# Kernel tuning notes

Hardware: AMD Instinct MI355X
Metric: run time of the kernel (lower is better)

## Reference

```python
import jax, jax.numpy as jnp
import numpy as np

DIM = 512
HEADS = 8
HEAD_DIM = DIM // HEADS
EPS = 1e-6
LN_EPS = 1e-5


def setup_inputs() -> dict:
    key = jax.random.key(0)
    ks = jax.random.split(key, 7)
    B, S = 2, 2048
    std = 1.0 / np.sqrt(DIM)
    return {
        "x": jax.random.normal(ks[0], (B, S, DIM), dtype=jnp.float32),
        "Wq": jax.random.normal(ks[1], (DIM, DIM), dtype=jnp.float32) * std,
        "Wk": jax.random.normal(ks[2], (DIM, DIM), dtype=jnp.float32) * std,
        "Wv": jax.random.normal(ks[3], (DIM, DIM), dtype=jnp.float32) * std,
        "Wo": jax.random.normal(ks[4], (DIM, DIM), dtype=jnp.float32) * std,
        "ln_gamma": jnp.ones((DIM,), dtype=jnp.float32),
        "ln_beta": jnp.zeros((DIM,), dtype=jnp.float32),
    }


def _hardsigmoid(x):
    return jnp.clip(x / 6.0 + 0.5, 0.0, 1.0)


def _softshrink(x, lambd=0.5):
    return jnp.where(x > lambd, x - lambd, jnp.where(x < -lambd, x + lambd, 0.0))


def reference(x, Wq, Wk, Wv, Wo, ln_gamma, ln_beta):
    B, S, D = x.shape
    # torch Linear: y = x @ W.T
    q = (x @ Wq.T).reshape(B, S, HEADS, HEAD_DIM).transpose(0, 2, 1, 3)
    k = (x @ Wk.T).reshape(B, S, HEADS, HEAD_DIM).transpose(0, 2, 1, 3)
    v = (x @ Wv.T).reshape(B, S, HEADS, HEAD_DIM).transpose(0, 2, 1, 3)
    scale = 1.0 / np.sqrt(HEAD_DIM)
    scores = jnp.einsum("bhqd,bhkd->bhqk", q, k) * scale  # [B,H,S,S]
    attn_soft = jax.nn.softmax(scores, axis=-1)
    gated = attn_soft * _hardsigmoid(scores)
    attn_weights = gated / (gated.sum(axis=-1, keepdims=True) + EPS)
    attn_out = jnp.einsum("bhqk,bhkd->bhqd", attn_weights, v)
    attn_out = attn_out.transpose(0, 2, 1, 3).reshape(B, S, D)
    out = attn_out @ Wo.T
    out = out / (1.0 + jnp.abs(out))  # softsign
    out = out + _softshrink(x)
    # LayerNorm over last dim
    mu = out.mean(axis=-1, keepdims=True)
    var = ((out - mu) ** 2).mean(axis=-1, keepdims=True)
    out = (out - mu) * jax.lax.rsqrt(var + LN_EPS) * ln_gamma + ln_beta
    return out
```

## Files before the change

### kernel.cpp

```cpp
#include <hip/hip_runtime.h>

#define DIMD 512
#define NB 2
#define SEQ 2048
#define NHEADS 8
#define HDIM 64
#define MROWS (NB*SEQ)

typedef short s16x8 __attribute__((ext_vector_type(8)));
typedef float f32x4 __attribute__((ext_vector_type(4)));
typedef float f32x16 __attribute__((ext_vector_type(16)));
typedef unsigned short u16;
typedef unsigned int u32;

__device__ __forceinline__ u16 f2bf(float f) {
    union { float f; u32 u; } c; c.f = f;
    u32 u = c.u;
    return (u16)((u + 0x7FFFu + ((u >> 16) & 1u)) >> 16);
}
__device__ __forceinline__ float bf2f(u16 v) {
    union { u32 u; float f; } c; c.u = ((u32)v) << 16;
    return c.f;
}

__device__ __forceinline__ f32x4 mfma16(s16x8 a, s16x8 b, f32x4 c) {
    return __builtin_amdgcn_mfma_f32_16x16x32_bf16(a, b, c, 0, 0, 0);
}
__device__ __forceinline__ f32x16 mfma32(s16x8 a, s16x8 b, f32x16 c) {
    return __builtin_amdgcn_mfma_f32_32x32x16_bf16(a, b, c, 0, 0, 0);
}
__device__ __forceinline__ float fexp2(float x) {
    float r; asm("v_exp_f32 %0, %1" : "=v"(r) : "v"(x)); return r;
}
__device__ __forceinline__ float frcp(float x) {
    float r; asm("v_rcp_f32 %0, %1" : "=v"(r) : "v"(x)); return r;
}

#define GLDS16(g, l) __builtin_amdgcn_global_load_lds( \
    (const __attribute__((address_space(1))) void*)(g), \
    (__attribute__((address_space(3))) void*)(l), 16, 0, 0)

#define ESCF 0.180336880111f
#define HSC2 0.115524530f

__global__ void cvt_all(const float* __restrict__ x, const float* __restrict__ Wq,
                        const float* __restrict__ Wk, const float* __restrict__ Wv,
                        const float* __restrict__ Wo,
                        u16* __restrict__ xb, u16* __restrict__ wqkv, u16* __restrict__ wo) {
    int i = blockIdx.x * blockDim.x + threadIdx.x;
    const float* src; u16* dst; int idx;
    if (i < 524288) { src = x; dst = xb; idx = i; }
    else {
        int jj = i - 524288;
        int which = jj >> 16; idx = jj & 65535;
        src = which == 0 ? Wq : which == 1 ? Wk : which == 2 ? Wv : Wo;
        dst = which < 3 ? wqkv + which*DIMD*DIMD : wo;
    }
    float4 v = reinterpret_cast<const float4*>(src)[idx];
    ushort4 o;
    o.x = f2bf(v.x); o.y = f2bf(v.y); o.z = f2bf(v.z); o.w = f2bf(v.w);
    reinterpret_cast<ushort4*>(dst)[idx] = o;
}

template<int WMODE>
__global__ __launch_bounds__(256) void gemm128(const u16* __restrict__ A, const u16* __restrict__ Bm,
                                               void* __restrict__ Cout, void* __restrict__ Cout2,
                                               void* __restrict__ Cout3, int M, int N, int K) {
    __shared__ u16 As[128*64];
    __shared__ u16 Bs[128*64];
    const int bm0 = blockIdx.x * 128, bn0 = blockIdx.y * 128;
    const int t = threadIdx.x;
    const int w = t >> 6, l = t & 63;
    const int lg = l >> 4, lr = l & 15;
    const int wm = w >> 1, wn = w & 1;
    f32x4 acc[4][4] = {};
    const int srow = w*32 + (l >> 3);
    const int swc = ((l & 7) ^ ((l >> 3) & 7)) * 8;
    const u16* asrc = A  + (size_t)(bm0 + srow)*K + swc;
    const u16* bsrc = Bm + (size_t)(bn0 + srow)*K + swc;
    const int ldsb = w*2048;

    for (int k0 = 0; k0 < K; k0 += 64) {
        #pragma unroll
        for (int g = 0; g < 4; g++) {
            GLDS16(asrc + (size_t)g*8*K + k0, &As[ldsb + g*512]);
            GLDS16(bsrc + (size_t)g*8*K + k0, &Bs[ldsb + g*512]);
        }
        __syncthreads();
        #pragma unroll
        for (int ks = 0; ks < 2; ks++) {
            const int swr = ((ks*4 + lg) ^ (lr & 7)) * 8;
            s16x8 af[4], bfr[4];
            #pragma unroll
            for (int fm = 0; fm < 4; fm++)
                af[fm] = *(const s16x8*)&As[(wm*64 + fm*16 + lr)*64 + swr];
            #pragma unroll
            for (int fn = 0; fn < 4; fn++)
                bfr[fn] = *(const s16x8*)&Bs[(wn*64 + fn*16 + lr)*64 + swr];
            #pragma unroll
            for (int fm = 0; fm < 4; fm++)
                #pragma unroll
                for (int fn = 0; fn < 4; fn++)
                    acc[fm][fn] = mfma16(af[fm], bfr[fn], acc[fm][fn]);
        }
        __syncthreads();
    }

    const int region = (WMODE == 3) ? (bn0 >> 9) : 0;
    const float qsc = (WMODE == 3 && region == 0) ? ESCF : 1.0f;
    #pragma unroll
    for (int fm = 0; fm < 4; fm++) {
        #pragma unroll
        for (int fn = 0; fn < 4; fn++) {
            const int mb = bm0 + wm*64 + fm*16 + lg*4;
            const int n  = bn0 + wn*64 + fn*16 + lr;
            if (WMODE == 2) {
                float* C = (float*)Cout;
                #pragma unroll
                for (int i = 0; i < 4; i++)
                    C[(size_t)(mb + i)*N + n] = acc[fm][fn][i];
            } else {
                const int nl = n & 511;
                if (region == 2) {
                    const int b = mb >> 11, s0 = mb & 2047;
                    const int h = nl >> 6, d = nl & 63;
                    ushort4 pk;
                    pk.x = f2bf(acc[fm][fn][0]);
                    pk.y = f2bf(acc[fm][fn][1]);
                    pk.z = f2bf(acc[fm][fn][2]);
                    pk.w = f2bf(acc[fm][fn][3]);
                    *(ushort4*)((u16*)Cout3 + (size_t)((b*8 + h)*64 + d)*2048 + s0) = pk;
                } else {
                    u16* C = region == 0 ? (u16*)Cout : (u16*)Cout2;
                    #pragma unroll
                    for (int i = 0; i < 4; i++)
                        C[(size_t)(mb + i)*512 + nl] = f2bf(acc[fm][fn][i] * qsc);
                }
            }
        }
    }
}

__global__ __launch_bounds__(256) void gemm_bt2f(const u16* __restrict__ opart,
                                                 const float* __restrict__ gpart,
                                                 const u16* __restrict__ Bm,
                                                 u16* __restrict__ Cout) {
    __shared__ u16 As[64*64];
    __shared__ u16 Bs[64*64];
    __shared__ float ginv[64][9];
    const int bm0 = blockIdx.x * 64, bn0 = blockIdx.y * 64;
    const int t = threadIdx.x;
    const int w = t >> 6, l = t & 63;
    const int lg = l >> 4, lr = l & 15;
    const int wm = w >> 1, wn = w & 1;
    f32x4 acc[2][2] = {};
    const int srow = t >> 3;
    const int c8 = t & 7;
    const int scol = c8 * 8;
    const int swz = (c8 ^ (srow & 7)) * 8;

    #pragma unroll
    for (int e = t; e < 512; e += 256) {
        const int r = e >> 3, h = e & 7;
        const int rg = bm0 + r;
        const int b = rg >> 11, s = rg & 2047;
        float g = gpart[(size_t)(b*8 + h)*SEQ + s]
                + gpart[(size_t)(16 + b*8 + h)*SEQ + s]
                + gpart[(size_t)(32 + b*8 + h)*SEQ + s]
                + gpart[(size_t)(48 + b*8 + h)*SEQ + s];
        ginv[r][h] = frcp(g);
    }
    __syncthreads();

    for (int k0 = 0; k0 < DIMD; k0 += 64) {
        const int h = k0 >> 6;
        #pragma unroll
        for (int c = 0; c < 2; c++) {
            const int rl = c*32 + srow;
            const int rg = bm0 + rl;
            const u16* gb = Bm + (size_t)(bn0 + rl)*DIMD + k0 + swz;
            GLDS16(gb, (char*)Bs + c*4096 + w*1024);
            const u16* oprow = opart + (size_t)rg*DIMD + k0 + scol;
            s16x8 p0 = *(const s16x8*)(oprow);
            s16x8 p1 = *(const s16x8*)(oprow + (size_t)MROWS*DIMD);
            s16x8 p2 = *(const s16x8*)(oprow + (size_t)2*MROWS*DIMD);
            s16x8 p3 = *(const s16x8*)(oprow + (size_t)3*MROWS*DIMD);
            const float inv = ginv[rl][h];
            union { u32 uu[4]; s16x8 v; } av;
            #pragma unroll
            for (int e2 = 0; e2 < 4; e2++) {
                const float s0 = (bf2f((u16)p0[2*e2]) + bf2f((u16)p1[2*e2]))
                               + (bf2f((u16)p2[2*e2]) + bf2f((u16)p3[2*e2]));
                const float s1 = (bf2f((u16)p0[2*e2+1]) + bf2f((u16)p1[2*e2+1]))
                               + (bf2f((u16)p2[2*e2+1]) + bf2f((u16)p3[2*e2+1]));
                asm("v_cvt_pk_bf16_f32 %0, %1, %2" : "=v"(av.uu[e2]) : "v"(s0*inv), "v"(s1*inv));
            }
            *(s16x8*)&As[rl*64 + swz] = av.v;
        }
        __syncthreads();
        #pragma unroll
        for (int ks = 0; ks < 2; ks++) {
            s16x8 af[2], bfr[2];
            const int rc = ((ks*4 + lg) ^ (lr & 7)) * 8;
            #pragma unroll
            for (int fm = 0; fm < 2; fm++)
                af[fm] = *(const s16x8*)&As[(wm*32 + fm*16 + lr)*64 + rc];
            #pragma unroll
            for (int fn = 0; fn < 2; fn++)
                bfr[fn] = *(const s16x8*)&Bs[(wn*32 + fn*16 + lr)*64 + rc];
            #pragma unroll
            for (int fm = 0; fm < 2; fm++)
                #pragma unroll
                for (int fn = 0; fn < 2; fn++)
                    acc[fm][fn] = mfma16(af[fm], bfr[fn], acc[fm][fn]);
        }
        __syncthreads();
    }

    #pragma unroll
    for (int fm = 0; fm < 2; fm++)
        #pragma unroll
        for (int fn = 0; fn < 2; fn++) {
            const int mb = bm0 + wm*32 + fm*16 + lg*4;
            const int n  = bn0 + wn*32 + fn*16 + lr;
            #pragma unroll
            for (int i = 0; i < 4; i++)
                Cout[(size_t)(mb + i)*DIMD + n] = f2bf(acc[fm][fn][i]);
        }
}

__device__ __forceinline__ void attn_phase64(const u16* Kc, const u16* Vc, const s16x8* qf,
                                             f32x16& o0, f32x16& o1, float& gacc,
                                             int ln, int hi, int l7) {
    f32x16 sc0 = {}, sc1 = {};
    __builtin_amdgcn_s_setprio(1);
    #pragma unroll
    for (int c = 0; c < 4; c++) {
        const int ch = (((c << 1) | hi) ^ l7) * 8;
        s16x8 kf0 = *(const s16x8*)&Kc[ln*64 + ch];
        s16x8 kf1 = *(const s16x8*)&Kc[(32 + ln)*64 + ch];
        sc0 = mfma32(kf0, qf[c], sc0);
        sc1 = mfma32(kf1, qf[c], sc1);
    }
    __builtin_amdgcn_s_setprio(0);
    #pragma unroll
    for (int kb = 0; kb < 2; kb++) {
        const f32x16& sc = kb ? sc1 : sc0;
        u32 u[4][2];
        #pragma unroll
        for (int b2 = 0; b2 < 4; b2++) {
            float ww[4];
            #pragma unroll
            for (int r = 0; r < 4; r++) {
                const float s = sc[b2*4 + r];
                const float e = fexp2(s);
                const float hs = __builtin_amdgcn_fmed3f(s*HSC2 + 0.5f, 0.f, 1.f);
                ww[r] = e*hs;
            }
            gacc += (ww[0] + ww[1]) + (ww[2] + ww[3]);
            asm("v_cvt_pk_bf16_f32 %0, %1, %2" : "=v"(u[b2][0]) : "v"(ww[0]), "v"(ww[1]));
            asm("v_cvt_pk_bf16_f32 %0, %1, %2" : "=v"(u[b2][1]) : "v"(ww[2]), "v"(ww[3]));
        }
        #pragma unroll
        for (int c16 = 0; c16 < 2; c16++) {
            u32 x0 = u[2*c16][0], y0 = u[2*c16+1][0];
            u32 x1 = u[2*c16][1], y1 = u[2*c16+1][1];
            asm("v_permlane32_swap_b32 %0, %1" : "+v"(x0), "+v"(y0));
            asm("v_permlane32_swap_b32 %0, %1" : "+v"(x1), "+v"(y1));
            union { u32 uu[4]; s16x8 v; } pa;
            pa.uu[0] = x0; pa.uu[1] = x1; pa.uu[2] = y0; pa.uu[3] = y1;
            const int ccv = kb*4 + c16*2 + hi;
            s16x8 vf0 = *(const s16x8*)&Vc[(size_t)ln*64        + (ccv ^ l7)*8];
            s16x8 vf1 = *(const s16x8*)&Vc[(size_t)(32 + ln)*64 + (ccv ^ l7)*8];
            __builtin_amdgcn_s_setprio(1);
            o0 = mfma32(pa.v, vf0, o0);
            o1 = mfma32(pa.v, vf1, o1);
            __builtin_amdgcn_s_setprio(0);
        }
    }
}

__global__ __launch_bounds__(256) void attn_split(const u16* __restrict__ q, const u16* __restrict__ k,
                                                  const u16* __restrict__ vt,
                                                  u16* __restrict__ opart, float* __restrict__ gpart) {
    __shared__ u16 Ks[2][64*64];
    __shared__ u16 Vs[2][64*64];
    const int bid = blockIdx.x;
    const int xcd = bid & 7, j = bid >> 3;
    const int g8 = j >> 4, qt = j & 15;
    const int bhks = xcd*8 + g8;
    const int bh = bhks >> 2, ks = bhks & 3;
    const int b = bh >> 3, h = bh & 7;
    const int qb0 = qt * 128;
    const int t = threadIdx.x;
    const int w = t >> 6, l = t & 63;
    const int ln = l & 31, hi = l >> 5, l7 = l & 7;

    const size_t qrow = (size_t)(b*SEQ + qb0 + w*32 + ln);
    s16x8 qf[4];
    #pragma unroll
    for (int c = 0; c < 4; c++)
        qf[c] = *(const s16x8*)(q + qrow*DIMD + h*HDIM + c*16 + hi*8);

    const int sr = l >> 3;
    const int swc = ((l & 7) ^ sr) * 8;
    const u16* ksrc = k  + (size_t)(b*SEQ + ks*512 + w*16 + sr)*DIMD + h*HDIM + swc;
    const u16* vsrc = vt + (size_t)bh*HDIM*SEQ + (size_t)(w*16 + sr)*SEQ + ks*512 + swc;
    const int ldsw = w*1024;

    f32x16 o0 = {}, o1 = {};
    float gacc = 0.f;

    #pragma unroll
    for (int g = 0; g < 2; g++) {
        GLDS16(ksrc + (size_t)g*8*DIMD, &Ks[0][ldsw + g*512]);
        GLDS16(vsrc + (size_t)g*8*SEQ,  &Vs[0][ldsw + g*512]);
    }
    __syncthreads();

    #pragma unroll 1
    for (int tp = 0; tp < 4; ++tp) {
        const int tt0 = tp*2;
        {
            const int adv = (tt0 + 1) * 64;
            #pragma unroll
            for (int g = 0; g < 2; g++) {
                GLDS16(ksrc + (size_t)(adv)*DIMD + (size_t)g*8*DIMD, &Ks[1][ldsw + g*512]);
                GLDS16(vsrc + (size_t)g*8*SEQ + adv,                 &Vs[1][ldsw + g*512]);
            }
        }
        attn_phase64(&Ks[0][0], &Vs[0][0], qf, o0, o1, gacc, ln, hi, l7);
        __syncthreads();
        if (tp < 3) {
            const int adv = (tt0 + 2) * 64;
            #pragma unroll
            for (int g = 0; g < 2; g++) {
                GLDS16(ksrc + (size_t)(adv)*DIMD + (size_t)g*8*DIMD, &Ks[0][ldsw + g*512]);
                GLDS16(vsrc + (size_t)g*8*SEQ + adv,                 &Vs[0][ldsw + g*512]);
            }
        }
        attn_phase64(&Ks[1][0], &Vs[1][0], qf, o0, o1, gacc, ln, hi, l7);
        __syncthreads();
    }

    gacc += __shfl_xor(gacc, 32);
    if (l < 32)
        gpart[((size_t)ks*16 + bh)*SEQ + qb0 + w*32 + l] = gacc;

    u16* op = opart + ((size_t)ks*MROWS + b*SEQ + qb0 + w*32)*DIMD + h*HDIM;
    #pragma unroll
    for (int i = 0; i < 16; i++) {
        const int qr = (i & 3) + 8*(i >> 2) + 4*hi;
        op[(size_t)qr*DIMD + ln]      = f2bf(o0[i]);
        op[(size_t)qr*DIMD + 32 + ln] = f2bf(o1[i]);
    }
}

__global__ __launch_bounds__(256) void ln_epilogue(const u16* __restrict__ proj, const float* __restrict__ x,
                                                   const float* __restrict__ gamma, const float* __restrict__ beta,
                                                   float* __restrict__ out) {
    const int row = blockIdx.x*4 + (threadIdx.x >> 6);
    const int l = threadIdx.x & 63;
    const u16* pr = proj + (size_t)row*DIMD + l*8;
    const float* xr = x  + (size_t)row*DIMD + l*8;
    s16x8 pv = *(const s16x8*)pr;
    float tv[8];
    float s = 0.f, s2 = 0.f;
    #pragma unroll
    for (int j = 0; j < 2; j++) {
        float4 xv = *(const float4*)(xr + j*4);
        float xa[4] = {xv.x, xv.y, xv.z, xv.w};
        #pragma unroll
        for (int qq = 0; qq < 4; qq++) {
            const float p = bf2f((u16)pv[j*4+qq]);
            const float ss = p / (1.f + fabsf(p));
            const float xx = xa[qq];
            const float sh = xx > 0.5f ? xx - 0.5f : (xx < -0.5f ? xx + 0.5f : 0.f);
            const float tt = ss + sh;
            tv[j*4+qq] = tt; s += tt; s2 += tt*tt;
        }
    }
    #pragma unroll
    for (int m = 1; m < 64; m <<= 1) { s += __shfl_xor(s, m); s2 += __shfl_xor(s2, m); }
    const float mu = s * (1.f/512.f);
    float var = s2 * (1.f/512.f) - mu*mu;
    const float rstd = rsqrtf(var + 1e-5f);
    #pragma unroll
    for (int j = 0; j < 2; j++) {
        float4 g  = *(const float4*)(gamma + l*8 + j*4);
        float4 bb = *(const float4*)(beta  + l*8 + j*4);
        float4 ov;
        ov.x = (tv[j*4+0]-mu)*rstd*g.x + bb.x;
        ov.y = (tv[j*4+1]-mu)*rstd*g.y + bb.y;
        ov.z = (tv[j*4+2]-mu)*rstd*g.z + bb.z;
        ov.w = (tv[j*4+3]-mu)*rstd*g.w + bb.w;
        *(float4*)(out + (size_t)row*DIMD + l*8 + j*4) = ov;
    }
}

extern "C" void kernel_launch(void* const* d_in, const int* in_sizes, int n_in,
                              void* d_out, int out_size, void* d_ws, size_t ws_size,
                              hipStream_t stream) {
    const float* x     = (const float*)d_in[0];
    const float* Wq    = (const float*)d_in[1];
    const float* Wk    = (const float*)d_in[2];
    const float* Wv    = (const float*)d_in[3];
    const float* Wo    = (const float*)d_in[4];
    const float* gamma = (const float*)d_in[5];
    const float* beta  = (const float*)d_in[6];
    float* out = (float*)d_out;
    char* ws = (char*)d_ws;

    u16* xb    = (u16*)(ws);
    u16* wqkvb = (u16*)(ws + (4<<20));
    u16* wob   = (u16*)(ws + (4<<20) + (1536<<10));
    u16* qb    = (u16*)(ws + (6<<20));
    u16* kb    = (u16*)(ws + (10<<20));
    u16* vtb   = (u16*)(ws + (14<<20));
    u16* proj  = (u16*)(ws + (22<<20));
    u16* opart = (u16*)(ws + (26<<20));
    float* gpart = (float*)(ws + (42<<20));

    cvt_all<<<3072, 256, 0, stream>>>(x, Wq, Wk, Wv, Wo, xb, wqkvb, wob);

    gemm128<3><<<dim3(MROWS/128, 1536/128), 256, 0, stream>>>(xb, wqkvb, qb, kb, vtb, MROWS, 1536, DIMD);

    attn_split<<<1024, 256, 0, stream>>>(qb, kb, vtb, opart, gpart);

    gemm_bt2f<<<dim3(MROWS/64, DIMD/64), 256, 0, stream>>>(opart, gpart, wob, proj);

    ln_epilogue<<<MROWS/4, 256, 0, stream>>>(proj, x, gamma, beta, out);
}
```

Baseline: 69.23 us.

## Load K/V fragments straight into registers instead of staging through LDS

The split-K attention kernel no longer stages K and V tiles in double-buffered shared memory. Each wave now loads its own MFMA fragments directly from global memory and handles its own 32-query tile, so the four waves in a block are independent and there are no block barriers. This removes the LDS traffic and __syncthreads, and the launch bounds ask for four blocks per CU to raise occupancy. In exchange, the four waves each fetch the same K/V data separately, which roughly quadruples global/L2 reads, and the loads are no longer overlapped with compute through explicit prefetch.

```diff
diff --git a/kernel.cpp b/kernel.cpp
--- a/kernel.cpp
+++ b/kernel.cpp
@@ -229,125 +229,90 @@
         }
 }
 
-__device__ __forceinline__ void attn_phase64(const u16* Kc, const u16* Vc, const s16x8* qf,
-                                             f32x16& o0, f32x16& o1, float& gacc,
-                                             int ln, int hi, int l7) {
-    f32x16 sc0 = {}, sc1 = {};
-    __builtin_amdgcn_s_setprio(1);
-    #pragma unroll
-    for (int c = 0; c < 4; c++) {
-        const int ch = (((c << 1) | hi) ^ l7) * 8;
-        s16x8 kf0 = *(const s16x8*)&Kc[ln*64 + ch];
-        s16x8 kf1 = *(const s16x8*)&Kc[(32 + ln)*64 + ch];
-        sc0 = mfma32(kf0, qf[c], sc0);
-        sc1 = mfma32(kf1, qf[c], sc1);
-    }
-    __builtin_amdgcn_s_setprio(0);
-    #pragma unroll
-    for (int kb = 0; kb < 2; kb++) {
-        const f32x16& sc = kb ? sc1 : sc0;
-        u32 u[4][2];
-        #pragma unroll
-        for (int b2 = 0; b2 < 4; b2++) {
-            float ww[4];
-            #pragma unroll
-            for (int r = 0; r < 4; r++) {
-                const float s = sc[b2*4 + r];
-                const float e = fexp2(s);
-                const float hs = __builtin_amdgcn_fmed3f(s*HSC2 + 0.5f, 0.f, 1.f);
-                ww[r] = e*hs;
-            }
-            gacc += (ww[0] + ww[1]) + (ww[2] + ww[3]);
-            asm("v_cvt_pk_bf16_f32 %0, %1, %2" : "=v"(u[b2][0]) : "v"(ww[0]), "v"(ww[1]));
-            asm("v_cvt_pk_bf16_f32 %0, %1, %2" : "=v"(u[b2][1]) : "v"(ww[2]), "v"(ww[3]));
-        }
-        #pragma unroll
-        for (int c16 = 0; c16 < 2; c16++) {
-            u32 x0 = u[2*c16][0], y0 = u[2*c16+1][0];
-            u32 x1 = u[2*c16][1], y1 = u[2*c16+1][1];
-            asm("v_permlane32_swap_b32 %0, %1" : "+v"(x0), "+v"(y0));
-            asm("v_permlane32_swap_b32 %0, %1" : "+v"(x1), "+v"(y1));
-            union { u32 uu[4]; s16x8 v; } pa;
-            pa.uu[0] = x0; pa.uu[1] = x1; pa.uu[2] = y0; pa.uu[3] = y1;
-            const int ccv = kb*4 + c16*2 + hi;
-            s16x8 vf0 = *(const s16x8*)&Vc[(size_t)ln*64        + (ccv ^ l7)*8];
-            s16x8 vf1 = *(const s16x8*)&Vc[(size_t)(32 + ln)*64 + (ccv ^ l7)*8];
-            __builtin_amdgcn_s_setprio(1);
-            o0 = mfma32(pa.v, vf0, o0);
-            o1 = mfma32(pa.v, vf1, o1);
-            __builtin_amdgcn_s_setprio(0);
-        }
-    }
-}
-
-__global__ __launch_bounds__(256) void attn_split(const u16* __restrict__ q, const u16* __restrict__ k,
-                                                  const u16* __restrict__ vt,
-                                                  u16* __restrict__ opart, float* __restrict__ gpart) {
-    __shared__ u16 Ks[2][64*64];
-    __shared__ u16 Vs[2][64*64];
+__global__ __launch_bounds__(256, 4) void attn_reg(const u16* __restrict__ q, const u16* __restrict__ k,
+                                                   const u16* __restrict__ vt,
+                                                   u16* __restrict__ opart, float* __restrict__ gpart) {
     const int bid = blockIdx.x;
     const int xcd = bid & 7, j = bid >> 3;
-    const int g8 = j >> 4, qt = j & 15;
-    const int bhks = xcd*8 + g8;
+    const int bhks = xcd*8 + (j >> 4);
     const int bh = bhks >> 2, ks = bhks & 3;
     const int b = bh >> 3, h = bh & 7;
-    const int qb0 = qt * 128;
-    const int t = threadIdx.x;
-    const int w = t >> 6, l = t & 63;
-    const int ln = l & 31, hi = l >> 5, l7 = l & 7;
-
-    const size_t qrow = (size_t)(b*SEQ + qb0 + w*32 + ln);
+    const int tid = threadIdx.x;
+    const int w = tid >> 6, l = tid & 63;
+    const int ln = l & 31, hi = l >> 5;
+    const int qt = (j & 15)*4 + w;
+    const int qb0 = qt * 32;
+
+    const size_t qrow = (size_t)(b*SEQ + qb0 + ln);
     s16x8 qf[4];
     #pragma unroll
     for (int c = 0; c < 4; c++)
         qf[c] = *(const s16x8*)(q + qrow*DIMD + h*HDIM + c*16 + hi*8);
 
-    const int sr = l >> 3;
-    const int swc = ((l & 7) ^ sr) * 8;
-    const u16* ksrc = k  + (size_t)(b*SEQ + ks*512 + w*16 + sr)*DIMD + h*HDIM + swc;
-    const u16* vsrc = vt + (size_t)bh*HDIM*SEQ + (size_t)(w*16 + sr)*SEQ + ks*512 + swc;
-    const int ldsw = w*1024;
+    const u16* kbp = k  + ((size_t)(b*SEQ + ks*512 + ln))*DIMD + h*HDIM + hi*8;
+    const u16* vbp = vt + (size_t)bh*HDIM*SEQ + (size_t)ln*SEQ + ks*512 + hi*8;
 
     f32x16 o0 = {}, o1 = {};
     float gacc = 0.f;
 
-    #pragma unroll
-    for (int g = 0; g < 2; g++) {
-        GLDS16(ksrc + (size_t)g*8*DIMD, &Ks[0][ldsw + g*512]);
-        GLDS16(vsrc + (size_t)g*8*SEQ,  &Vs[0][ldsw + g*512]);
-    }
-    __syncthreads();
-
     #pragma unroll 1
-    for (int tp = 0; tp < 4; ++tp) {
-        const int tt0 = tp*2;
-        {
-            const int adv = (tt0 + 1) * 64;
-            #pragma unroll
-            for (int g = 0; g < 2; g++) {
-                GLDS16(ksrc + (size_t)(adv)*DIMD + (size_t)g*8*DIMD, &Ks[1][ldsw + g*512]);
-                GLDS16(vsrc + (size_t)g*8*SEQ + adv,                 &Vs[1][ldsw + g*512]);
+    for (int tp = 0; tp < 8; ++tp) {
+        #pragma unroll
+        for (int kb = 0; kb < 2; kb++) {
+            const int key0 = tp*64 + kb*32;
+            const u16* kp = kbp + (size_t)key0*DIMD;
+            const u16* vp = vbp + key0;
+            s16x8 kf0 = *(const s16x8*)(kp);
+            s16x8 kf1 = *(const s16x8*)(kp + 16);
+            s16x8 kf2 = *(const s16x8*)(kp + 32);
+            s16x8 kf3 = *(const s16x8*)(kp + 48);
+            s16x8 vfa = *(const s16x8*)(vp);
+            s16x8 vfb = *(const s16x8*)(vp + 16);
+            s16x8 vfc = *(const s16x8*)(vp + (size_t)32*SEQ);
+            s16x8 vfd = *(const s16x8*)(vp + (size_t)32*SEQ + 16);
+            f32x16 sc = {};
+            __builtin_amdgcn_s_setprio(1);
+            sc = mfma32(kf0, qf[0], sc);
+            sc = mfma32(kf1, qf[1], sc);
+            sc = mfma32(kf2, qf[2], sc);
+            sc = mfma32(kf3, qf[3], sc);
+            __builtin_amdgcn_s_setprio(0);
+            u32 u[4][2];
+            #pragma unroll
+            for (int b2 = 0; b2 < 4; b2++) {
+                float ww[4];
+                #pragma unroll
+                for (int r = 0; r < 4; r++) {
+                    const float s = sc[b2*4 + r];
+                    const float e = fexp2(s);
+                    const float hs = __builtin_amdgcn_fmed3f(s*HSC2 + 0.5f, 0.f, 1.f);
+                    ww[r] = e*hs;
+                }
+                gacc += (ww[0] + ww[1]) + (ww[2] + ww[3]);
+                asm("v_cvt_pk_bf16_f32 %0, %1, %2" : "=v"(u[b2][0]) : "v"(ww[0]), "v"(ww[1]));
+                asm("v_cvt_pk_bf16_f32 %0, %1, %2" : "=v"(u[b2][1]) : "v"(ww[2]), "v"(ww[3]));
             }
-        }
-        attn_phase64(&Ks[0][0], &Vs[0][0], qf, o0, o1, gacc, ln, hi, l7);
-        __syncthreads();
-        if (tp < 3) {
-            const int adv = (tt0 + 2) * 64;
-            #pragma unroll
-            for (int g = 0; g < 2; g++) {
-                GLDS16(ksrc + (size_t)(adv)*DIMD + (size_t)g*8*DIMD, &Ks[0][ldsw + g*512]);
-                GLDS16(vsrc + (size_t)g*8*SEQ + adv,                 &Vs[0][ldsw + g*512]);
+            #pragma unroll
+            for (int c16 = 0; c16 < 2; c16++) {
+                u32 x0 = u[2*c16][0], y0 = u[2*c16+1][0];
+                u32 x1 = u[2*c16][1], y1 = u[2*c16+1][1];
+                asm("v_permlane32_swap_b32 %0, %1" : "+v"(x0), "+v"(y0));
+                asm("v_permlane32_swap_b32 %0, %1" : "+v"(x1), "+v"(y1));
+                union { u32 uu[4]; s16x8 v; } pa;
+                pa.uu[0] = x0; pa.uu[1] = x1; pa.uu[2] = y0; pa.uu[3] = y1;
+                __builtin_amdgcn_s_setprio(1);
+                o0 = mfma32(pa.v, c16 ? vfb : vfa, o0);
+                o1 = mfma32(pa.v, c16 ? vfd : vfc, o1);
+                __builtin_amdgcn_s_setprio(0);
             }
         }
-        attn_phase64(&Ks[1][0], &Vs[1][0], qf, o0, o1, gacc, ln, hi, l7);
-        __syncthreads();
     }
 
     gacc += __shfl_xor(gacc, 32);
     if (l < 32)
-        gpart[((size_t)ks*16 + bh)*SEQ + qb0 + w*32 + l] = gacc;
-
-    u16* op = opart + ((size_t)ks*MROWS + b*SEQ + qb0 + w*32)*DIMD + h*HDIM;
+        gpart[((size_t)ks*16 + bh)*SEQ + qb0 + l] = gacc;
+
+    u16* op = opart + ((size_t)ks*MROWS + b*SEQ + qb0)*DIMD + h*HDIM;
     #pragma unroll
     for (int i = 0; i < 16; i++) {
         const int qr = (i & 3) + 8*(i >> 2) + 4*hi;
@@ -425,7 +390,7 @@
 
     gemm128<3><<<dim3(MROWS/128, 1536/128), 256, 0, stream>>>(xb, wqkvb, qb, kb, vtb, MROWS, 1536, DIMD);
 
-    attn_split<<<1024, 256, 0, stream>>>(qb, kb, vtb, opart, gpart);
+    attn_reg<<<1024, 256, 0, stream>>>(qb, kb, vtb, opart, gpart);
 
     gemm_bt2f<<<dim3(MROWS/64, DIMD/64), 256, 0, stream>>>(opart, gpart, wob, proj);
 
```

New measurement: 104.7 us. +51.2%, slower.
